# Optimization experiments

Measured on AMD Instinct MI355X. Metric: run time of the kernel, lower is better.

Reference implementation:

```python
import jax, jax.numpy as jnp
import numpy as np

N_HEAD = 12

def setup_inputs() -> dict:
    key = jax.random.key(0)
    k1, k2, k3 = jax.random.split(key, 3)
    B, T, C = 4, 2048, 768
    x = jax.random.normal(k1, (B, T, C), dtype=jnp.float32)
    # c_attn params (Linear(n_embd, 3*n_embd)); stored as [in, out] for x @ W
    W_attn = jax.random.normal(k2, (C, 3 * C), dtype=jnp.float32) * (1.0 / np.sqrt(C))
    b_attn = jax.random.normal(k3, (3 * C,), dtype=jnp.float32) * 0.02
    return {"x": x, "W_attn": W_attn, "b_attn": b_attn}

def reference(x, W_attn, b_attn):
    B, T, C = x.shape
    H = N_HEAD
    Dh = C // H
    qkv = x @ W_attn + b_attn                      # [B,T,3C]
    q, k, v = jnp.split(qkv, 3, axis=-1)
    q = q.reshape(B, T, H, Dh)
    k = k.reshape(B, T, H, Dh)
    v = v.reshape(B, T, H, Dh)
    scale = 1.0 / np.sqrt(Dh)
    # scaled QK^T per head: [B,H,T,T]
    scores = jnp.einsum('bqhd,bkhd->bhqk', q * scale, k)
    causal = jnp.tril(jnp.ones((T, T), dtype=bool))  # [T,T]
    # masked-to--inf then ReLU == zero out non-causal and clamp at 0
    p = jnp.where(causal, jnp.maximum(scores, 0.0), 0.0)
    y = jnp.einsum('bhqk,bkhd->bqhd', p, v).reshape(B, T, C)
    return y
```

## Files before the change

### kernel.cpp

```cpp
#include <hip/hip_runtime.h>
#include <cstdint>
#include <cstddef>

typedef unsigned short u16;
typedef unsigned int u32;
typedef unsigned long long u64;
typedef __bf16 bf16x8 __attribute__((ext_vector_type(8)));
typedef float f32x4 __attribute__((ext_vector_type(4)));

__device__ __forceinline__ u16 f2bf(float f) {
    unsigned int x = __builtin_bit_cast(unsigned int, f);
    x += 0x7FFFu + ((x >> 16) & 1u);
    return (u16)(x >> 16);
}

__device__ __forceinline__ bf16x8 ldfrag(const u16* p) {
    bf16x8 r;
    __builtin_memcpy(&r, (const u16*)__builtin_assume_aligned(p, 16), 16);
    return r;
}

__device__ __forceinline__ void async16(u16* lds, const u16* g) {
    __builtin_amdgcn_global_load_lds(
        (const __attribute__((address_space(1))) void*)g,
        (__attribute__((address_space(3))) void*)lds,
        16, 0, 0);
}

__global__ __launch_bounds__(256) void prep(const float* __restrict__ x,
                                            u16* __restrict__ xb,
                                            const float* __restrict__ W,
                                            u16* __restrict__ Wt) {
    const int bx = blockIdx.x;
    if (bx < 6144) {
        const int i = (bx * 256 + threadIdx.x) * 4;
        float4 v = *reinterpret_cast<const float4*>(x + i);
        union { u16 e[4]; u64 u; } w;
        w.e[0] = f2bf(v.x); w.e[1] = f2bf(v.y); w.e[2] = f2bf(v.z); w.e[3] = f2bf(v.w);
        *reinterpret_cast<u64*>(xb + i) = w.u;
    } else {
        const int R = 768, Ccols = 2304;
        __shared__ float tile[32][33];
        const int bb = bx - 6144;
        const int bxc = (bb % 72) * 32;
        const int byr = (bb / 72) * 32;
        const int tx = threadIdx.x & 31, ty = threadIdx.x >> 5;
        #pragma unroll
        for (int i = 0; i < 32; i += 8)
            tile[ty + i][tx] = W[(size_t)(byr + ty + i) * Ccols + bxc + tx];
        __syncthreads();
        #pragma unroll
        for (int i = 0; i < 32; i += 8)
            Wt[(size_t)(bxc + ty + i) * R + byr + tx] = f2bf(tile[tx][ty + i]);
    }
}

__global__ __launch_bounds__(256) void qkv_gemm(const u16* __restrict__ A,
                                                const u16* __restrict__ Bt,
                                                const float* __restrict__ bias,
                                                u16* __restrict__ qk,
                                                u16* __restrict__ Vt) {
    const int N = 2304, K = 768, QKW = 1536;
    __shared__ __align__(16) u16 sA[2][128 * 32];
    __shared__ __align__(16) u16 sB[2][128 * 32];
    const int t = threadIdx.x;
    const int wave = t >> 6, lane = t & 63;
    const int quad = lane >> 4, l16 = lane & 15;
    const int wr = wave >> 1, wc = wave & 1;
    const int m0 = blockIdx.y * 128, n0 = blockIdx.x * 128;

    const int srow = wave * 32 + (lane >> 2);
    const int sseg = lane & 3;

    f32x4 acc[4][4] = {};

    auto stage = [&](int k0, int bi) {
        #pragma unroll
        for (int j = 0; j < 2; ++j) {
            const int row = srow + j * 16;
            async16(&sA[bi][0] + wave * 1024 + j * 512,
                    A + (size_t)(m0 + row) * K + k0 + sseg * 8);
            async16(&sB[bi][0] + wave * 1024 + j * 512,
                    Bt + (size_t)(n0 + row) * K + k0 + sseg * 8);
        }
    };

    stage(0, 0);
    __syncthreads();

    int buf = 0;
    for (int k0 = 0; k0 < K; k0 += 32) {
        if (k0 + 32 < K) stage(k0 + 32, buf ^ 1);

        bf16x8 af[4], bfr[4];
        #pragma unroll
        for (int i = 0; i < 4; ++i)
            af[i] = ldfrag(&sA[buf][0] + (wr * 64 + i * 16 + l16) * 32 + quad * 8);
        #pragma unroll
        for (int j = 0; j < 4; ++j)
            bfr[j] = ldfrag(&sB[buf][0] + (wc * 64 + j * 16 + l16) * 32 + quad * 8);
        #pragma unroll
        for (int i = 0; i < 4; ++i)
            #pragma unroll
            for (int j = 0; j < 4; ++j)
                acc[i][j] = __builtin_amdgcn_mfma_f32_16x16x32_bf16(af[i], bfr[j], acc[i][j], 0, 0, 0);

        __syncthreads();
        buf ^= 1;
    }

    if (n0 < 1536) {
        #pragma unroll
        for (int i = 0; i < 4; ++i)
            #pragma unroll
            for (int j = 0; j < 4; ++j) {
                const int col = n0 + wc * 64 + j * 16 + l16;
                const float bc = bias[col];
                const float scale = (col < 768) ? 0.125f : 1.0f;
                #pragma unroll
                for (int r = 0; r < 4; ++r) {
                    const int row = m0 + wr * 64 + i * 16 + quad * 4 + r;
                    qk[(size_t)row * QKW + col] = f2bf((acc[i][j][r] + bc) * scale);
                }
            }
    } else {
        const int h = ((n0 - 1536) >> 6) + wc;
        #pragma unroll
        for (int i = 0; i < 4; ++i) {
            const int grow = m0 + wr * 64 + i * 16 + quad * 4;
            const int b = grow >> 11, tok = grow & 2047;
            #pragma unroll
            for (int j = 0; j < 4; ++j) {
                const int d = j * 16 + l16;
                const float bc = bias[1536 + h * 64 + d];
                u32 lo = (u32)f2bf(acc[i][j][0] + bc) | ((u32)f2bf(acc[i][j][1] + bc) << 16);
                u32 hi = (u32)f2bf(acc[i][j][2] + bc) | ((u32)f2bf(acc[i][j][3] + bc) << 16);
                u64 pk = (u64)lo | ((u64)hi << 32);
                *reinterpret_cast<u64*>(Vt + ((size_t)((b * 12 + h) * 64 + d)) * 2048 + tok) = pk;
            }
        }
    }
}

__global__ __launch_bounds__(256, 3) void attn_kernel(const u16* __restrict__ qk,
                                                      const u16* __restrict__ Vt,
                                                      float* __restrict__ out) {
    const int T = 2048, QKW = 1536, Cc = 768, Dh = 64;

    const int bid = blockIdx.x;
    const int rr = bid >> 8;
    const int ss = bid & 255;
    const int x = ss & 15;
    const int qa = (rr == 0) ? x : (rr == 1) ? (15 - x) : ((x + 8) & 15);
    const int qb = 31 - qa;
    const int hb = (ss >> 4) + (rr << 4);
    const int h = hb % 12, b = hb / 12;

    const int t = threadIdx.x;
    const int wave = t >> 6, lane = t & 63;
    const int quad = lane >> 4, l16 = lane & 15;

    __shared__ __align__(16) u16 sK[2][64 * 64];
    __shared__ __align__(16) u16 sV[2][64 * 64];
    __shared__ __align__(16) u16 sP[128 * 72];

    const u16* qbase = qk + (size_t)b * T * QKW + (size_t)h * Dh;
    const u16* kbase = qbase + 768;
    const u16* vtb = Vt + (size_t)(b * 12 + h) * 64 * 2048;

    bf16x8 qf[8][2];
    #pragma unroll
    for (int cg = 0; cg < 8; ++cg) {
        const int qrow = ((cg < 4) ? qa * 64 : (qb * 64 - 64)) + cg * 16 + l16;
        const u16* p = qbase + (size_t)qrow * QKW + quad * 8;
        qf[cg][0] = ldfrag(p);
        qf[cg][1] = ldfrag(p + 32);
    }

    f32x4 oacc[2][4] = {};

    const int srow = wave * 8 + (lane >> 3);
    const int sch = (lane & 7) ^ ((lane >> 3) & 7);

    auto stageK = [&](int it, int bi) {
        #pragma unroll
        for (int j = 0; j < 2; ++j)
            async16(&sK[bi][0] + j * 2048 + wave * 512,
                    kbase + (size_t)(it * 64 + j * 32 + srow) * QKW + sch * 8);
    };
    auto stageV = [&](int it, int bi) {
        #pragma unroll
        for (int j = 0; j < 2; ++j)
            async16(&sV[bi][0] + j * 2048 + wave * 512,
                    vtb + (size_t)(j * 32 + srow) * 2048 + it * 64 + sch * 8);
    };

    stageK(0, 0);
    stageV(0, 0);
    __syncthreads();

    int buf = 0;
    for (int it = 0; it <= qb; ++it) {
        const bool more = (it < qb);
        if (more) stageK(it + 1, buf ^ 1);

        const bool act_a = (it <= qa);

        bf16x8 kf0, kf1;
        {
            const u16* kr = &sK[buf][0] + (wave * 16 + l16) * 64;
            const int rsw = l16 & 7;
            kf0 = ldfrag(kr + ((quad ^ rsw) << 3));
            kf1 = ldfrag(kr + (((quad + 4) ^ rsw) << 3));
        }
        const int cg_lo = act_a ? 0 : 4;
        #pragma unroll
        for (int cg = 7; cg >= 0; --cg) {
            if (cg < cg_lo) break;
            f32x4 s = {};
            s = __builtin_amdgcn_mfma_f32_16x16x32_bf16(kf0, qf[cg][0], s, 0, 0, 0);
            s = __builtin_amdgcn_mfma_f32_16x16x32_bf16(kf1, qf[cg][1], s, 0, 0, 0);
            const bool diag = (cg < 4) ? (it == qa) : (it == qb);
            u32 bits[4];
            #pragma unroll
            for (int r = 0; r < 4; ++r) {
                float v = fmaxf(s[r], 0.0f);
                if (diag && (wave * 16 + quad * 4 + r > (cg & 3) * 16 + l16)) v = 0.0f;
                bits[r] = __builtin_bit_cast(u32, v);
            }
            u32 pk[2];
            pk[0] = (bits[1] & 0xFFFF0000u) | (bits[0] >> 16);
            pk[1] = (bits[3] & 0xFFFF0000u) | (bits[2] >> 16);
            __builtin_memcpy((u16*)__builtin_assume_aligned(
                                 sP + (cg * 16 + l16) * 72 + wave * 16 + quad * 4, 8),
                             pk, 8);
        }
        __syncthreads();

        if (more) stageV(it + 1, buf ^ 1);

        #pragma unroll
        for (int kk = 0; kk < 2; ++kk) {
            bf16x8 ap1 = ldfrag(sP + (64 + wave * 16 + l16) * 72 + kk * 32 + quad * 8);
            bf16x8 ap0;
            if (act_a) ap0 = ldfrag(sP + (wave * 16 + l16) * 72 + kk * 32 + quad * 8);
            #pragma unroll
            for (int dt = 0; dt < 4; ++dt) {
                const int d = dt * 16 + l16;
                bf16x8 bv = ldfrag(&sV[buf][0] + d * 64 + (((kk * 4 + quad) ^ (l16 & 7)) << 3));
                oacc[1][dt] = __builtin_amdgcn_mfma_f32_16x16x32_bf16(ap1, bv, oacc[1][dt], 0, 0, 0);
                if (act_a)
                    oacc[0][dt] = __builtin_amdgcn_mfma_f32_16x16x32_bf16(ap0, bv, oacc[0][dt], 0, 0, 0);
            }
        }

        __syncthreads();
        buf ^= 1;
    }

    #pragma unroll
    for (int g = 0; g < 2; ++g)
        #pragma unroll
        for (int dt = 0; dt < 4; ++dt)
            #pragma unroll
            for (int r = 0; r < 4; ++r) {
                const int tok = (g == 0 ? qa * 64 : qb * 64) + wave * 16 + quad * 4 + r;
                const int c = h * Dh + dt * 16 + l16;
                out[((size_t)b * T + tok) * Cc + c] = oacc[g][dt][r];
            }
}

extern "C" void kernel_launch(void* const* d_in, const int* in_sizes, int n_in,
                              void* d_out, int out_size, void* d_ws, size_t ws_size,
                              hipStream_t stream) {
    const float* x    = (const float*)d_in[0];
    const float* W    = (const float*)d_in[1];
    const float* bias = (const float*)d_in[2];
    float* out = (float*)d_out;

    char* ws = (char*)d_ws;
    const size_t xb_bytes = (size_t)8192 * 768 * 2;
    const size_t wt_bytes = (size_t)2304 * 768 * 2;
    const size_t qk_bytes = (size_t)8192 * 1536 * 2;
    u16* xb = (u16*)ws;
    u16* Wt = (u16*)(ws + xb_bytes);
    u16* qk = (u16*)(ws + xb_bytes + wt_bytes);
    u16* Vt = (u16*)(ws + xb_bytes + wt_bytes + qk_bytes);

    prep<<<6144 + 1728, 256, 0, stream>>>(x, xb, W, Wt);
    qkv_gemm<<<dim3(18, 64), 256, 0, stream>>>(xb, Wt, bias, qk, Vt);
    attn_kernel<<<768, 256, 0, stream>>>(qk, Vt, out);
}
```

Before: 199.6 us.

## Single-buffer LDS tiles to raise attention occupancy; drop GEMM double buffering

Both the QKV GEMM and the attention kernel switch from double-buffered to single-buffered LDS tiles. In attention, the next K tile is now prefetched once the score phase has finished reading sK, and the next V tile once the PV phase has finished reading sV. This cuts LDS use per block, so launch bounds go from 3 to 4 blocks per SM to hide latency with more resident waves. The GEMM now loads a tile, synchronises and computes with no overlap, which exposes global-load latency on every K step.

```diff
diff --git a/kernel.cpp b/kernel.cpp
--- a/kernel.cpp
+++ b/kernel.cpp
@@ -61,8 +61,8 @@
                                                 u16* __restrict__ qk,
                                                 u16* __restrict__ Vt) {
     const int N = 2304, K = 768, QKW = 1536;
-    __shared__ __align__(16) u16 sA[2][128 * 32];
-    __shared__ __align__(16) u16 sB[2][128 * 32];
+    __shared__ __align__(16) u16 sA[128 * 32];
+    __shared__ __align__(16) u16 sB[128 * 32];
     const int t = threadIdx.x;
     const int wave = t >> 6, lane = t & 63;
     const int quad = lane >> 4, l16 = lane & 15;
@@ -74,39 +74,30 @@
 
     f32x4 acc[4][4] = {};
 
-    auto stage = [&](int k0, int bi) {
+    for (int k0 = 0; k0 < K; k0 += 32) {
+        __syncthreads();
         #pragma unroll
         for (int j = 0; j < 2; ++j) {
             const int row = srow + j * 16;
-            async16(&sA[bi][0] + wave * 1024 + j * 512,
+            async16(sA + wave * 1024 + j * 512,
                     A + (size_t)(m0 + row) * K + k0 + sseg * 8);
-            async16(&sB[bi][0] + wave * 1024 + j * 512,
+            async16(sB + wave * 1024 + j * 512,
                     Bt + (size_t)(n0 + row) * K + k0 + sseg * 8);
         }
-    };
-
-    stage(0, 0);
-    __syncthreads();
-
-    int buf = 0;
-    for (int k0 = 0; k0 < K; k0 += 32) {
-        if (k0 + 32 < K) stage(k0 + 32, buf ^ 1);
+        __syncthreads();
 
         bf16x8 af[4], bfr[4];
         #pragma unroll
         for (int i = 0; i < 4; ++i)
-            af[i] = ldfrag(&sA[buf][0] + (wr * 64 + i * 16 + l16) * 32 + quad * 8);
+            af[i] = ldfrag(sA + (wr * 64 + i * 16 + l16) * 32 + quad * 8);
         #pragma unroll
         for (int j = 0; j < 4; ++j)
-            bfr[j] = ldfrag(&sB[buf][0] + (wc * 64 + j * 16 + l16) * 32 + quad * 8);
+            bfr[j] = ldfrag(sB + (wc * 64 + j * 16 + l16) * 32 + quad * 8);
         #pragma unroll
         for (int i = 0; i < 4; ++i)
             #pragma unroll
             for (int j = 0; j < 4; ++j)
                 acc[i][j] = __builtin_amdgcn_mfma_f32_16x16x32_bf16(af[i], bfr[j], acc[i][j], 0, 0, 0);
-
-        __syncthreads();
-        buf ^= 1;
     }
 
     if (n0 < 1536) {
@@ -142,7 +133,7 @@
     }
 }
 
-__global__ __launch_bounds__(256, 3) void attn_kernel(const u16* __restrict__ qk,
+__global__ __launch_bounds__(256, 4) void attn_kernel(const u16* __restrict__ qk,
                                                       const u16* __restrict__ Vt,
                                                       float* __restrict__ out) {
     const int T = 2048, QKW = 1536, Cc = 768, Dh = 64;
@@ -160,8 +151,8 @@
     const int wave = t >> 6, lane = t & 63;
     const int quad = lane >> 4, l16 = lane & 15;
 
-    __shared__ __align__(16) u16 sK[2][64 * 64];
-    __shared__ __align__(16) u16 sV[2][64 * 64];
+    __shared__ __align__(16) u16 sK[64 * 64];
+    __shared__ __align__(16) u16 sV[64 * 64];
     __shared__ __align__(16) u16 sP[128 * 72];
 
     const u16* qbase = qk + (size_t)b * T * QKW + (size_t)h * Dh;
@@ -182,33 +173,30 @@
     const int srow = wave * 8 + (lane >> 3);
     const int sch = (lane & 7) ^ ((lane >> 3) & 7);
 
-    auto stageK = [&](int it, int bi) {
+    auto stageK = [&](int it) {
         #pragma unroll
         for (int j = 0; j < 2; ++j)
-            async16(&sK[bi][0] + j * 2048 + wave * 512,
+            async16(sK + j * 2048 + wave * 512,
                     kbase + (size_t)(it * 64 + j * 32 + srow) * QKW + sch * 8);
     };
-    auto stageV = [&](int it, int bi) {
+    auto stageV = [&](int it) {
         #pragma unroll
         for (int j = 0; j < 2; ++j)
-            async16(&sV[bi][0] + j * 2048 + wave * 512,
+            async16(sV + j * 2048 + wave * 512,
                     vtb + (size_t)(j * 32 + srow) * 2048 + it * 64 + sch * 8);
     };
 
-    stageK(0, 0);
-    stageV(0, 0);
+    stageK(0);
+    stageV(0);
     __syncthreads();
 
-    int buf = 0;
     for (int it = 0; it <= qb; ++it) {
         const bool more = (it < qb);
-        if (more) stageK(it + 1, buf ^ 1);
-
         const bool act_a = (it <= qa);
 
         bf16x8 kf0, kf1;
         {
-            const u16* kr = &sK[buf][0] + (wave * 16 + l16) * 64;
+            const u16* kr = sK + (wave * 16 + l16) * 64;
             const int rsw = l16 & 7;
             kf0 = ldfrag(kr + ((quad ^ rsw) << 3));
             kf1 = ldfrag(kr + (((quad + 4) ^ rsw) << 3));
@@ -237,7 +225,7 @@
         }
         __syncthreads();
 
-        if (more) stageV(it + 1, buf ^ 1);
+        if (more) stageK(it + 1);
 
         #pragma unroll
         for (int kk = 0; kk < 2; ++kk) {
@@ -247,15 +235,15 @@
             #pragma unroll
             for (int dt = 0; dt < 4; ++dt) {
                 const int d = dt * 16 + l16;
-                bf16x8 bv = ldfrag(&sV[buf][0] + d * 64 + (((kk * 4 + quad) ^ (l16 & 7)) << 3));
+                bf16x8 bv = ldfrag(sV + d * 64 + (((kk * 4 + quad) ^ (l16 & 7)) << 3));
                 oacc[1][dt] = __builtin_amdgcn_mfma_f32_16x16x32_bf16(ap1, bv, oacc[1][dt], 0, 0, 0);
                 if (act_a)
                     oacc[0][dt] = __builtin_amdgcn_mfma_f32_16x16x32_bf16(ap0, bv, oacc[0][dt], 0, 0, 0);
             }
         }
-
-        __syncthreads();
-        buf ^= 1;
+        __syncthreads();
+
+        if (more) stageV(it + 1);
     }
 
     #pragma unroll
```

After: 191.9 us. 1.04x faster.
